# Kernel optimization log

Hardware: AMD Instinct MI355X
Metric: run time of the kernel (lower is better)

Reference implementation:

```python
import jax, jax.numpy as jnp
import numpy as np

HEADS = 8

def setup_inputs() -> dict:
    key = jax.random.key(0)
    ks = jax.random.split(key, 5)
    B, C, H, W = 2, 256, 64, 64
    dim = C
    x = jax.random.normal(ks[0], (B, C, H, W), dtype=jnp.float32)
    # Linear weights stored as [in, out] so y = x @ W + b
    w_qkv = jax.random.normal(ks[1], (dim, 3 * dim), dtype=jnp.float32) * (dim ** -0.5)
    b_qkv = jax.random.normal(ks[2], (3 * dim,), dtype=jnp.float32) * 0.02
    w_out = jax.random.normal(ks[3], (dim, dim), dtype=jnp.float32) * (dim ** -0.5)
    b_out = jax.random.normal(ks[4], (dim,), dtype=jnp.float32) * 0.02
    return {"x": x, "w_qkv": w_qkv, "b_qkv": b_qkv, "w_out": w_out, "b_out": b_out}

def reference(x, w_qkv, b_qkv, w_out, b_out):
    B, C, H, W = x.shape
    h = HEADS
    d = C // h
    scale = d ** -0.5
    # [B, C, H, W] -> [B, N, C]
    tokens = x.reshape(B, C, H * W).transpose(0, 2, 1)
    qkv = tokens @ w_qkv + b_qkv  # [B, N, 3C]
    q, k, v = jnp.split(qkv, 3, axis=-1)
    def to_heads(t):
        Bn, N, _ = t.shape
        return t.reshape(Bn, N, h, d).transpose(0, 2, 1, 3)  # [B, h, N, d]
    q, k, v = map(to_heads, (q, k, v))
    dots = jnp.einsum('bhnd,bhmd->bhnm', q, k) * scale  # [B, h, N, N]
    attn = jax.nn.softmax(dots, axis=-1)
    out = jnp.einsum('bhnm,bhmd->bhnd', attn, v)  # [B, h, N, d]
    out = out.transpose(0, 2, 1, 3).reshape(B, H * W, C)  # [B, N, C]
    out = out @ w_out + b_out
    return out.transpose(0, 2, 1).reshape(B, C, H, W)
```

## Files before the change

### kernel.cpp

```cpp
#include <hip/hip_runtime.h>

typedef __attribute__((ext_vector_type(8))) short s16x8;
typedef __attribute__((ext_vector_type(4))) float f32x4;
typedef __attribute__((ext_vector_type(16))) float f32x16;
typedef __attribute__((ext_vector_type(2))) unsigned u32x2;
typedef __attribute__((ext_vector_type(4))) unsigned u32x4;

#define MFMA32(a, b, c) __builtin_amdgcn_mfma_f32_16x16x32_bf16((a), (b), (c), 0, 0, 0)

#if __has_builtin(__builtin_amdgcn_mfma_f32_32x32x16_bf16)
#define MFMA3216(a, b, c) __builtin_amdgcn_mfma_f32_32x32x16_bf16((a), (b), (c), 0, 0, 0)
#else
#define MFMA3216(a, b, c) (c)
#endif

#if __has_builtin(__builtin_amdgcn_exp2f)
#define EXP2F(x) __builtin_amdgcn_exp2f(x)
#else
#define EXP2F(x) __exp2f(x)
#endif

#if __has_builtin(__builtin_amdgcn_rcpf)
#define RCPF(x) __builtin_amdgcn_rcpf(x)
#else
#define RCPF(x) (1.0f / (x))
#endif

#define SL2E 0.25507313f

__device__ __forceinline__ unsigned pkrne(float a, float b) {
  unsigned ua = __builtin_bit_cast(unsigned, a);
  unsigned ub = __builtin_bit_cast(unsigned, b);
  ua += 0x7FFFu + ((ua >> 16) & 1u);
  ub += 0x7FFFu + ((ub >> 16) & 1u);
  return __builtin_amdgcn_perm(ub, ua, 0x07060302u);
}

__device__ __forceinline__ unsigned pktrunc(float a, float b) {
  return __builtin_amdgcn_perm(__builtin_bit_cast(unsigned, b),
                               __builtin_bit_cast(unsigned, a), 0x07060302u);
}

__device__ __forceinline__ unsigned short bfr(float f) {
  unsigned u = __builtin_bit_cast(unsigned, f);
  u += 0x7FFFu + ((u >> 16) & 1u);
  return (unsigned short)(u >> 16);
}

__device__ __forceinline__ float bflo(unsigned u) {
  return __builtin_bit_cast(float, u << 16);
}
__device__ __forceinline__ float bfhi(unsigned u) {
  return __builtin_bit_cast(float, u & 0xFFFF0000u);
}

__device__ __forceinline__ u32x2 plswap(unsigned a, unsigned b) {
#if __has_builtin(__builtin_amdgcn_permlane32_swap)
  return __builtin_amdgcn_permlane32_swap(a, b, false, false);
#else
  unsigned sa = (unsigned)__shfl_xor((int)a, 32, 64);
  unsigned sb = (unsigned)__shfl_xor((int)b, 32, 64);
  bool hi = (threadIdx.x & 63) >= 32;
  u32x2 r;
  r.x = hi ? sb : a;
  r.y = hi ? b : sa;
  return r;
#endif
}

__device__ __forceinline__ void stage16(const ushort* g, ushort* l, int lane) {
#if __has_builtin(__builtin_amdgcn_global_load_lds)
  __builtin_amdgcn_global_load_lds(
      (__attribute__((address_space(1))) unsigned int*)(unsigned long long)(
          const void*)g,
      (__attribute__((address_space(3))) unsigned int*)(unsigned)(
          unsigned long long)(const void*)l,
      16, 0, 0);
#else
  *(uint4*)(l + lane * 8) = *(const uint4*)g;
#endif
}

__global__ __launch_bounds__(256) void prep_kernel(
    const float* __restrict__ x, const float* __restrict__ wqkv,
    const float* __restrict__ wout, ushort* __restrict__ xbf,
    ushort* __restrict__ wT, ushort* __restrict__ woT) {
  const int t = threadIdx.x;
  const int sub = t & 15, grp = t >> 4;
  const int id = blockIdx.x;
  const float* src;
  ushort* dst;
  int src_ld, k0, n0;
  float sc = 1.f;
  if (id < 512) {
    int mt = id & 63, kt = (id >> 6) & 3, b = id >> 8;
    src = x + (size_t)b * 256 * 4096;
    src_ld = 4096;
    dst = xbf + (size_t)b * 4096 * 256;
    k0 = kt * 64;
    n0 = mt * 64;
  } else if (id < 560) {
    int r = id - 512, nt = r % 12, kt = r / 12;
    src = wqkv;
    src_ld = 768;
    dst = wT;
    k0 = kt * 64;
    n0 = nt * 64;
    if (n0 < 256) sc = SL2E;
  } else {
    int r = id - 560, nt = r & 3, kt = r >> 2;
    src = wout;
    src_ld = 256;
    dst = woT;
    k0 = kt * 64;
    n0 = nt * 64;
  }
  const int k = k0 + grp * 4;
  const int n = n0 + sub * 4;
  unsigned d0[4], d1[4];
#pragma unroll
  for (int i = 0; i < 4; ++i) {
    float4 v = *(const float4*)(src + (size_t)(k + i) * src_ld + n);
    d0[i] = pkrne(v.x * sc, v.y * sc);
    d1[i] = pkrne(v.z * sc, v.w * sc);
  }
  u32x2 r0 = {__builtin_amdgcn_perm(d0[1], d0[0], 0x05040100u),
              __builtin_amdgcn_perm(d0[3], d0[2], 0x05040100u)};
  u32x2 r1 = {__builtin_amdgcn_perm(d0[1], d0[0], 0x07060302u),
              __builtin_amdgcn_perm(d0[3], d0[2], 0x07060302u)};
  u32x2 r2 = {__builtin_amdgcn_perm(d1[1], d1[0], 0x05040100u),
              __builtin_amdgcn_perm(d1[3], d1[2], 0x05040100u)};
  u32x2 r3 = {__builtin_amdgcn_perm(d1[1], d1[0], 0x07060302u),
              __builtin_amdgcn_perm(d1[3], d1[2], 0x07060302u)};
  *(u32x2*)(dst + (size_t)(n + 0) * 256 + k) = r0;
  *(u32x2*)(dst + (size_t)(n + 1) * 256 + k) = r1;
  *(u32x2*)(dst + (size_t)(n + 2) * 256 + k) = r2;
  *(u32x2*)(dst + (size_t)(n + 3) * 256 + k) = r3;
}

__global__ __launch_bounds__(256) void qkv_kernel(
    const ushort* __restrict__ xbf, const ushort* __restrict__ wT,
    const float* __restrict__ bq, ushort* __restrict__ QG,
    ushort* __restrict__ KG, ushort* __restrict__ VtG) {
  __shared__ __align__(16) ushort Wl[64][40];
  __shared__ __align__(16) ushort Xl[128][40];
  const int t0 = blockIdx.x * 128;
  const int n0 = blockIdx.y * 64;
  const int t = threadIdx.x;
  const int wid = t >> 6, lane = t & 63;
  const int wy = wid >> 1, wx = wid & 1;
  const int quad = lane >> 4, l16 = lane & 15;
  f32x4 acc[2][4] = {};
  const int wr = t >> 2, wsg = t & 3;
  for (int k0 = 0; k0 < 256; k0 += 32) {
    __syncthreads();
    *(uint4*)&Wl[wr][wsg * 8] =
        *(const uint4*)(wT + (size_t)(n0 + wr) * 256 + k0 + wsg * 8);
#pragma unroll
    for (int i = 0; i < 2; ++i) {
      int fid = t + 256 * i, row = fid >> 2, seg = fid & 3;
      *(uint4*)&Xl[row][seg * 8] =
          *(const uint4*)(xbf + (size_t)(t0 + row) * 256 + k0 + seg * 8);
    }
    __syncthreads();
    s16x8 wf[2], xf[4];
#pragma unroll
    for (int i = 0; i < 2; ++i)
      wf[i] = *(const s16x8*)&Wl[32 * wy + 16 * i + l16][quad * 8];
#pragma unroll
    for (int j = 0; j < 4; ++j)
      xf[j] = *(const s16x8*)&Xl[64 * wx + 16 * j + l16][quad * 8];
#pragma unroll
    for (int i = 0; i < 2; ++i)
#pragma unroll
      for (int j = 0; j < 4; ++j) acc[i][j] = MFMA32(wf[i], xf[j], acc[i][j]);
  }
  if (n0 < 256) {
#pragma unroll
    for (int i = 0; i < 2; ++i) {
      int nb = n0 + 32 * wy + 16 * i + 4 * quad;
      float4 b4 = *(const float4*)(bq + nb);
      float bx0 = b4.x * SL2E, bx1 = b4.y * SL2E, bx2 = b4.z * SL2E,
            bx3 = b4.w * SL2E;
      int h = ((nb & 255) >> 5);
      int dd0 = nb & 31;
#pragma unroll
      for (int j = 0; j < 4; ++j) {
        int tok = t0 + 64 * wx + 16 * j + l16;
        int b = tok >> 12, tokn = tok & 4095;
        u32x2 pk = {pkrne(acc[i][j][0] + bx0, acc[i][j][1] + bx1),
                    pkrne(acc[i][j][2] + bx2, acc[i][j][3] + bx3)};
        *(u32x2*)(QG + ((size_t)(b * 8 + h) * 4096 + tokn) * 32 + dd0) = pk;
      }
    }
  } else if (n0 < 512) {
#pragma unroll
    for (int i = 0; i < 2; ++i) {
      int nb = n0 + 32 * wy + 16 * i + 4 * quad;
      float4 b4 = *(const float4*)(bq + nb);
      float bx0 = b4.x, bx1 = b4.y, bx2 = b4.z, bx3 = b4.w;
      int h = ((nb & 255) >> 5);
      size_t fo = (size_t)i * 512 + (quad >> 1) * 256 + (quad & 1) * 4;
#pragma unroll
      for (int j = 0; j < 4; ++j) {
        int tok = t0 + 64 * wx + 16 * j + l16;
        int b = tok >> 12, tokn = tok & 4095;
        int tl = tokn >> 6, ss = (tokn >> 5) & 1, l5 = tokn & 31;
        u32x2 pk = {pkrne(acc[i][j][0] + bx0, acc[i][j][1] + bx1),
                    pkrne(acc[i][j][2] + bx2, acc[i][j][3] + bx3)};
        *(u32x2*)(KG + (size_t)(b * 8 + h) * 131072 + (size_t)tl * 2048 +
                  ss * 1024 + l5 * 8 + fo) = pk;
      }
    }
  } else {
#pragma unroll
    for (int i = 0; i < 2; ++i) {
      int nb = n0 + 32 * wy + 16 * i + 4 * quad;
      float4 b4 = *(const float4*)(bq + nb);
      float bb[4] = {b4.x, b4.y, b4.z, b4.w};
#pragma unroll
      for (int r = 0; r < 4; ++r) {
        int nn = nb + r - 512;
        int h = nn >> 5, d = nn & 31;
#pragma unroll
        for (int j = 0; j < 4; ++j) {
          int tok = t0 + 64 * wx + 16 * j + l16;
          int b = tok >> 12, tokn = tok & 4095;
          int tl = tokn >> 6, ss = (tokn >> 5) & 1;
          int hV = (tokn >> 4) & 1, hii = (tokn >> 3) & 1, e = tokn & 7;
          VtG[(size_t)(b * 8 + h) * 131072 + (size_t)tl * 2048 + ss * 1024 +
              hV * 512 + hii * 256 + d * 8 + e] = bfr(acc[i][j][r] + bb[r]);
        }
      }
    }
  }
}

struct AttnAcc {
  f32x16 o;
  f32x16 o_l;
};

__device__ __forceinline__ void softpv(const f32x16& S, const ushort* vhalf,
                                       int lane, f32x16& o, f32x16& o_l) {
  const s16x8 ones8 = {(short)0x3F80, (short)0x3F80, (short)0x3F80,
                       (short)0x3F80, (short)0x3F80, (short)0x3F80,
                       (short)0x3F80, (short)0x3F80};
  unsigned w8[8];
#pragma unroll
  for (int ii = 0; ii < 8; ++ii)
    w8[ii] = pktrunc(EXP2F(S[2 * ii]), EXP2F(S[2 * ii + 1]));
  u32x2 sw0 = plswap(w8[0], w8[2]);
  u32x2 sw1 = plswap(w8[1], w8[3]);
  u32x2 sw2 = plswap(w8[4], w8[6]);
  u32x2 sw3 = plswap(w8[5], w8[7]);
  u32x4 pa0 = {sw0.x, sw1.x, sw0.y, sw1.y};
  u32x4 pa1 = {sw2.x, sw3.x, sw2.y, sw3.y};
  const s16x8 pA0 = __builtin_bit_cast(s16x8, pa0);
  const s16x8 pA1 = __builtin_bit_cast(s16x8, pa1);
  const s16x8 va0 = *(const s16x8*)(vhalf + lane * 8);
  const s16x8 va1 = *(const s16x8*)(vhalf + 512 + lane * 8);
  o = MFMA3216(pA0, va0, o);
  o = MFMA3216(pA1, va1, o);
  o_l = MFMA3216(pA0, ones8, o_l);
  o_l = MFMA3216(pA1, ones8, o_l);
}

__global__ __launch_bounds__(256, 4) void attn_split(
    const ushort* __restrict__ QG, const ushort* __restrict__ KG,
    const ushort* __restrict__ VtG, ushort* __restrict__ OF0,
    ushort* __restrict__ OFb, float* __restrict__ LF) {
  __shared__ __align__(64) ushort KVs[3][4096];
  const int id = blockIdx.x;
  const int bh = (id & 7) * 2 + ((id >> 3) & 1);
  const int q0 = ((id >> 4) & 31) * 128;
  const int sp = id >> 9;
  const int kt0 = sp * 32;
  const int niter = 32;
  const int t = threadIdx.x;
  const int wid = t >> 6, lane = t & 63;
  const int l5 = lane & 31, hi = lane >> 5;
  const ushort* qp = QG + (size_t)bh * 4096 * 32;
  const ushort* kgp = KG + (size_t)bh * 131072 + (size_t)kt0 * 2048;
  const ushort* vgp = VtG + (size_t)bh * 131072 + (size_t)kt0 * 2048;
  const int qw = q0 + 32 * wid;
  const ushort* qrow = qp + (size_t)(qw + l5) * 32 + hi * 8;
  const s16x8 qf0 = *(const s16x8*)(qrow);
  const s16x8 qf1 = *(const s16x8*)(qrow + 16);
  const int kdst = wid * 512;
  const ushort* kpre = kgp + kdst + lane * 8;
  const ushort* vpre = vgp + kdst + lane * 8;
  stage16(kpre, &KVs[0][kdst], lane);
  stage16(vpre, &KVs[0][2048 + kdst], lane);
  kpre += 2048;
  vpre += 2048;
  __syncthreads();
  f32x16 o = {};
  f32x16 o_l = {};
  f32x16 S1p = {};
  int b = 0, bm1 = 2, bp1 = 1;
  const int lo8 = lane * 8;
  for (int i = 0; i < niter; ++i) {
    if (i + 1 < niter) {
      stage16(kpre, &KVs[bp1][kdst], lane);
      stage16(vpre, &KVs[bp1][2048 + kdst], lane);
      kpre += 2048;
      vpre += 2048;
    }
    const ushort* kb = &KVs[b][0];
    const s16x8 ka00 = *(const s16x8*)(kb + lo8);
    const s16x8 ka01 = *(const s16x8*)(kb + 512 + lo8);
    f32x16 S0 = {};
    S0 = MFMA3216(ka00, qf0, S0);
    S0 = MFMA3216(ka01, qf1, S0);
    if (i > 0) softpv(S1p, &KVs[bm1][2048 + 1024], lane, o, o_l);
    const s16x8 ka10 = *(const s16x8*)(kb + 1024 + lo8);
    const s16x8 ka11 = *(const s16x8*)(kb + 1536 + lo8);
    f32x16 S1 = {};
    S1 = MFMA3216(ka10, qf0, S1);
    S1 = MFMA3216(ka11, qf1, S1);
    softpv(S0, &KVs[b][2048], lane, o, o_l);
    S1p = S1;
    __syncthreads();
    bm1 = b;
    b = bp1;
    bp1 = (bp1 + 1 == 3) ? 0 : bp1 + 1;
  }
  softpv(S1p, &KVs[bm1][2048 + 1024], lane, o, o_l);
  ushort* OFs = (sp == 0) ? OF0 : OFb;
  float* LFs = LF + (size_t)sp * 65536;
#pragma unroll
  for (int r = 0; r < 16; ++r) {
    int q = qw + (r & 3) + 8 * (r >> 2) + 4 * hi;
    OFs[((size_t)bh * 4096 + q) * 32 + l5] = bfr(o[r]);
  }
  float lval = o_l[0];
#pragma unroll
  for (int r = 1; r < 16; ++r) lval = (l5 == r) ? o_l[r] : lval;
  if (l5 < 16)
    LFs[(size_t)bh * 4096 + qw + (l5 & 3) + 8 * (l5 >> 2) + 4 * hi] = lval;
}

__global__ __launch_bounds__(256) void proj_split(
    const ushort* __restrict__ OF0, const ushort* __restrict__ OFb,
    const float* __restrict__ LF, const ushort* __restrict__ woT,
    const float* __restrict__ bo, float* __restrict__ out) {
  __shared__ __align__(16) ushort Wl[64][40];
  __shared__ __align__(16) ushort Xl[64][40];
  const int t0 = blockIdx.x * 64;
  const int c0 = blockIdx.y * 64;
  const int t = threadIdx.x;
  const int wid = t >> 6, lane = t & 63;
  const int wy = wid >> 1, wx = wid & 1;
  const int quad = lane >> 4, l16 = lane & 15;
  f32x4 acc[2][2] = {};
  const int wr = t >> 2, wsg = t & 3;
  const int c8 = (t & 7) * 4;
  for (int k0 = 0; k0 < 256; k0 += 32) {
    __syncthreads();
    *(uint4*)&Wl[wr][wsg * 8] =
        *(const uint4*)(woT + (size_t)(c0 + wr) * 256 + k0 + wsg * 8);
    const int hh = k0 >> 5;
#pragma unroll
    for (int p = 0; p < 2; ++p) {
      int row = 32 * p + (t >> 3);
      int tok = t0 + row, bb = tok >> 12, tokn = tok & 4095;
      size_t ro = (size_t)(bb * 8 + hh) * 4096 + tokn;
      size_t oi = ro * 32 + c8;
      uint2 a0 = *(const uint2*)(OF0 + oi);
      uint2 a1 = *(const uint2*)(OFb + oi);
      float l = LF[ro] + LF[65536 + ro];
      float inv = RCPF(l);
      f32x4 s;
      s[0] = bflo(a0.x) + bflo(a1.x);
      s[1] = bfhi(a0.x) + bfhi(a1.x);
      s[2] = bflo(a0.y) + bflo(a1.y);
      s[3] = bfhi(a0.y) + bfhi(a1.y);
      s *= inv;
      u32x2 pk = {pkrne(s[0], s[1]), pkrne(s[2], s[3])};
      *(u32x2*)&Xl[row][c8] = pk;
    }
    __syncthreads();
    s16x8 wf[2], xf[2];
#pragma unroll
    for (int i = 0; i < 2; ++i)
      wf[i] = *(const s16x8*)&Wl[32 * wy + 16 * i + l16][quad * 8];
#pragma unroll
    for (int j = 0; j < 2; ++j)
      xf[j] = *(const s16x8*)&Xl[32 * wx + 16 * j + l16][quad * 8];
#pragma unroll
    for (int i = 0; i < 2; ++i)
#pragma unroll
      for (int j = 0; j < 2; ++j) acc[i][j] = MFMA32(wf[i], xf[j], acc[i][j]);
  }
#pragma unroll
  for (int i = 0; i < 2; ++i) {
    int cb = c0 + 32 * wy + 16 * i + 4 * quad;
    float4 b4 = *(const float4*)(bo + cb);
    float bb[4] = {b4.x, b4.y, b4.z, b4.w};
#pragma unroll
    for (int j = 0; j < 2; ++j) {
      int tok = t0 + 32 * wx + 16 * j + l16;
      int b = tok >> 12, tokn = tok & 4095;
#pragma unroll
      for (int r = 0; r < 4; ++r)
        out[((size_t)(b * 256 + cb + r)) * 4096 + tokn] = acc[i][j][r] + bb[r];
    }
  }
}

extern "C" void kernel_launch(void* const* d_in, const int* in_sizes, int n_in,
                              void* d_out, int out_size, void* d_ws, size_t ws_size,
                              hipStream_t stream) {
  (void)in_sizes; (void)n_in; (void)out_size; (void)ws_size;
  const float* x = (const float*)d_in[0];
  const float* wq = (const float*)d_in[1];
  const float* bq = (const float*)d_in[2];
  const float* wo = (const float*)d_in[3];
  const float* bo = (const float*)d_in[4];
  float* out = (float*)d_out;
  ushort* ws = (ushort*)d_ws;
  ushort* xbf = ws;
  ushort* OF0 = ws;
  ushort* QG  = ws + 2097152;
  ushort* KG  = ws + 4194304;
  ushort* VtG = ws + 6291456;
  ushort* wT  = ws + 8388608;
  ushort* woT = ws + 8585216;
  ushort* OFb = ws + 8650752;
  float* LF = (float*)(ws + 12845056);
  prep_kernel<<<576, 256, 0, stream>>>(x, wq, wo, xbf, wT, woT);
  qkv_kernel<<<dim3(64, 12), 256, 0, stream>>>(xbf, wT, bq, QG, KG, VtG);
  attn_split<<<1024, 256, 0, stream>>>(QG, KG, VtG, OF0, OFb, LF);
  proj_split<<<dim3(128, 4), 256, 0, stream>>>(OF0, OFb, LF, woT, bo, out);
}
```

Measured before the change: 136.6 us.

## Quad-buffer K/V tiles with explicit vmcnt waits and unrolled attention loop

Replaces the triple-buffered K/V loop with a 4-deep LDS ring, fully unrolled in groups of four so buffer indices are compile-time constants. Each step waits on the global loads with explicit s_waitcnt vmcnt counts and a raw s_barrier, which lets one stage of prefetch stay in flight across the barrier instead of draining everything at __syncthreads. It also raises wave priority around the QK MFMAs. In exchange, LDS use per block grows by a third, which may limit occupancy, and correctness now depends on the hand-written waitcnt values matching what stage16 actually issues.

```diff
diff --git a/kernel.cpp b/kernel.cpp
--- a/kernel.cpp
+++ b/kernel.cpp
@@ -236,11 +236,6 @@
   }
 }
 
-struct AttnAcc {
-  f32x16 o;
-  f32x16 o_l;
-};
-
 __device__ __forceinline__ void softpv(const f32x16& S, const ushort* vhalf,
                                        int lane, f32x16& o, f32x16& o_l) {
   const s16x8 ones8 = {(short)0x3F80, (short)0x3F80, (short)0x3F80,
@@ -266,17 +261,48 @@
   o_l = MFMA3216(pA1, ones8, o_l);
 }
 
+#define ATTN_STEP(CUR, PRV, SKEW, LAST)                                      \
+  {                                                                          \
+    if (!(LAST)) {                                                           \
+      stage16(kpre, &KVs[((CUR) + 1) & 3][kdst], lane);                      \
+      stage16(vpre, &KVs[((CUR) + 1) & 3][2048 + kdst], lane);               \
+      kpre += 2048;                                                          \
+      vpre += 2048;                                                          \
+      asm volatile("s_waitcnt vmcnt(2)" ::: "memory");                       \
+    } else {                                                                 \
+      asm volatile("s_waitcnt vmcnt(0)" ::: "memory");                       \
+    }                                                                        \
+    __builtin_amdgcn_sched_barrier(0);                                       \
+    __builtin_amdgcn_s_barrier();                                            \
+    __builtin_amdgcn_sched_barrier(0);                                       \
+    const ushort* kb = &KVs[(CUR)][0];                                       \
+    const s16x8 ka00 = *(const s16x8*)(kb + lo8);                            \
+    const s16x8 ka01 = *(const s16x8*)(kb + 512 + lo8);                      \
+    __builtin_amdgcn_s_setprio(1);                                           \
+    f32x16 S0 = MFMA3216(ka00, qf0, fz);                                     \
+    S0 = MFMA3216(ka01, qf1, S0);                                            \
+    __builtin_amdgcn_s_setprio(0);                                           \
+    if (SKEW) softpv(S1p, &KVs[(PRV)][2048 + 1024], lane, o, o_l);           \
+    const s16x8 ka10 = *(const s16x8*)(kb + 1024 + lo8);                     \
+    const s16x8 ka11 = *(const s16x8*)(kb + 1536 + lo8);                     \
+    __builtin_amdgcn_s_setprio(1);                                           \
+    f32x16 S1 = MFMA3216(ka10, qf0, fz);                                     \
+    S1 = MFMA3216(ka11, qf1, S1);                                            \
+    __builtin_amdgcn_s_setprio(0);                                           \
+    softpv(S0, &KVs[(CUR)][2048], lane, o, o_l);                             \
+    S1p = S1;                                                                \
+  }
+
 __global__ __launch_bounds__(256, 4) void attn_split(
     const ushort* __restrict__ QG, const ushort* __restrict__ KG,
     const ushort* __restrict__ VtG, ushort* __restrict__ OF0,
     ushort* __restrict__ OFb, float* __restrict__ LF) {
-  __shared__ __align__(64) ushort KVs[3][4096];
+  __shared__ __align__(64) ushort KVs[4][4096];
   const int id = blockIdx.x;
   const int bh = (id & 7) * 2 + ((id >> 3) & 1);
   const int q0 = ((id >> 4) & 31) * 128;
   const int sp = id >> 9;
   const int kt0 = sp * 32;
-  const int niter = 32;
   const int t = threadIdx.x;
   const int wid = t >> 6, lane = t & 63;
   const int l5 = lane & 31, hi = lane >> 5;
@@ -294,39 +320,26 @@
   stage16(vpre, &KVs[0][2048 + kdst], lane);
   kpre += 2048;
   vpre += 2048;
-  __syncthreads();
   f32x16 o = {};
   f32x16 o_l = {};
   f32x16 S1p = {};
-  int b = 0, bm1 = 2, bp1 = 1;
+  const f32x16 fz = {};
   const int lo8 = lane * 8;
-  for (int i = 0; i < niter; ++i) {
-    if (i + 1 < niter) {
-      stage16(kpre, &KVs[bp1][kdst], lane);
-      stage16(vpre, &KVs[bp1][2048 + kdst], lane);
-      kpre += 2048;
-      vpre += 2048;
-    }
-    const ushort* kb = &KVs[b][0];
-    const s16x8 ka00 = *(const s16x8*)(kb + lo8);
-    const s16x8 ka01 = *(const s16x8*)(kb + 512 + lo8);
-    f32x16 S0 = {};
-    S0 = MFMA3216(ka00, qf0, S0);
-    S0 = MFMA3216(ka01, qf1, S0);
-    if (i > 0) softpv(S1p, &KVs[bm1][2048 + 1024], lane, o, o_l);
-    const s16x8 ka10 = *(const s16x8*)(kb + 1024 + lo8);
-    const s16x8 ka11 = *(const s16x8*)(kb + 1536 + lo8);
-    f32x16 S1 = {};
-    S1 = MFMA3216(ka10, qf0, S1);
-    S1 = MFMA3216(ka11, qf1, S1);
-    softpv(S0, &KVs[b][2048], lane, o, o_l);
-    S1p = S1;
-    __syncthreads();
-    bm1 = b;
-    b = bp1;
-    bp1 = (bp1 + 1 == 3) ? 0 : bp1 + 1;
-  }
-  softpv(S1p, &KVs[bm1][2048 + 1024], lane, o, o_l);
+  ATTN_STEP(0, 3, false, false)
+  ATTN_STEP(1, 0, true, false)
+  ATTN_STEP(2, 1, true, false)
+  ATTN_STEP(3, 2, true, false)
+  for (int g = 1; g < 7; ++g) {
+    ATTN_STEP(0, 3, true, false)
+    ATTN_STEP(1, 0, true, false)
+    ATTN_STEP(2, 1, true, false)
+    ATTN_STEP(3, 2, true, false)
+  }
+  ATTN_STEP(0, 3, true, false)
+  ATTN_STEP(1, 0, true, false)
+  ATTN_STEP(2, 1, true, false)
+  ATTN_STEP(3, 2, true, true)
+  softpv(S1p, &KVs[3][2048 + 1024], lane, o, o_l);
   ushort* OFs = (sp == 0) ? OF0 : OFb;
   float* LFs = LF + (size_t)sp * 65536;
 #pragma unroll
```

Result: no change. 134.9 us (-1.2%).

## Pre-swizzle X and weights into fragment-tiled layout, use direct-to-LDS loads with double buffering

Applied to the files above, without the earlier changes.

The prep kernel now writes bf16 X and weight matrices in a tiled layout that matches the MFMA fragment order. This lets the QKV and projection GEMMs stage tiles with global_load_lds, and the QKV GEMM double-buffers them so the next k-slice loads during compute. The attention kernel drops from a triple-buffered software pipeline with a deferred softmax·V stage to a simpler double-buffered loop, unrolled two tiles per iteration. The aim is to cut register-staged LDS writes and padding overhead. The cost is less overlap inside each attention iteration.

```diff
diff --git a/kernel.cpp b/kernel.cpp
--- a/kernel.cpp
+++ b/kernel.cpp
@@ -81,6 +81,15 @@
 #endif
 }
 
+__device__ __forceinline__ size_t flX(int n, int k) {
+  return (size_t)(n >> 7) * 32768 + (size_t)(k >> 5) * 4096 +
+         ((n >> 4) & 7) * 512 + ((k >> 3) & 3) * 128 + (n & 15) * 8 + (k & 7);
+}
+__device__ __forceinline__ size_t flW(int n, int k) {
+  return (size_t)(n >> 6) * 16384 + (size_t)(k >> 5) * 2048 +
+         ((n >> 4) & 3) * 512 + ((k >> 3) & 3) * 128 + (n & 15) * 8 + (k & 7);
+}
+
 __global__ __launch_bounds__(256) void prep_kernel(
     const float* __restrict__ x, const float* __restrict__ wqkv,
     const float* __restrict__ wout, ushort* __restrict__ xbf,
@@ -91,14 +100,16 @@
   const float* src;
   ushort* dst;
   int src_ld, k0, n0;
+  bool isX = false;
   float sc = 1.f;
   if (id < 512) {
     int mt = id & 63, kt = (id >> 6) & 3, b = id >> 8;
     src = x + (size_t)b * 256 * 4096;
     src_ld = 4096;
-    dst = xbf + (size_t)b * 4096 * 256;
+    dst = xbf + (size_t)b * 1048576;
     k0 = kt * 64;
     n0 = mt * 64;
+    isX = true;
   } else if (id < 560) {
     int r = id - 512, nt = r % 12, kt = r / 12;
     src = wqkv;
@@ -132,48 +143,60 @@
               __builtin_amdgcn_perm(d1[3], d1[2], 0x05040100u)};
   u32x2 r3 = {__builtin_amdgcn_perm(d1[1], d1[0], 0x07060302u),
               __builtin_amdgcn_perm(d1[3], d1[2], 0x07060302u)};
-  *(u32x2*)(dst + (size_t)(n + 0) * 256 + k) = r0;
-  *(u32x2*)(dst + (size_t)(n + 1) * 256 + k) = r1;
-  *(u32x2*)(dst + (size_t)(n + 2) * 256 + k) = r2;
-  *(u32x2*)(dst + (size_t)(n + 3) * 256 + k) = r3;
+  if (isX) {
+    *(u32x2*)(dst + flX(n + 0, k)) = r0;
+    *(u32x2*)(dst + flX(n + 1, k)) = r1;
+    *(u32x2*)(dst + flX(n + 2, k)) = r2;
+    *(u32x2*)(dst + flX(n + 3, k)) = r3;
+  } else {
+    *(u32x2*)(dst + flW(n + 0, k)) = r0;
+    *(u32x2*)(dst + flW(n + 1, k)) = r1;
+    *(u32x2*)(dst + flW(n + 2, k)) = r2;
+    *(u32x2*)(dst + flW(n + 3, k)) = r3;
+  }
 }
 
 __global__ __launch_bounds__(256) void qkv_kernel(
     const ushort* __restrict__ xbf, const ushort* __restrict__ wT,
     const float* __restrict__ bq, ushort* __restrict__ QG,
     ushort* __restrict__ KG, ushort* __restrict__ VtG) {
-  __shared__ __align__(16) ushort Wl[64][40];
-  __shared__ __align__(16) ushort Xl[128][40];
+  __shared__ __align__(64) ushort WL[2][2048];
+  __shared__ __align__(64) ushort XL[2][4096];
   const int t0 = blockIdx.x * 128;
   const int n0 = blockIdx.y * 64;
   const int t = threadIdx.x;
   const int wid = t >> 6, lane = t & 63;
   const int wy = wid >> 1, wx = wid & 1;
   const int quad = lane >> 4, l16 = lane & 15;
+  const int lo8 = lane * 8;
   f32x4 acc[2][4] = {};
-  const int wr = t >> 2, wsg = t & 3;
-  for (int k0 = 0; k0 < 256; k0 += 32) {
+  const ushort* wsrc = wT + (size_t)blockIdx.y * 16384 + wid * 512 + lo8;
+  const ushort* xsrc = xbf + (size_t)blockIdx.x * 32768 + wid * 1024 + lo8;
+  stage16(wsrc, &WL[0][wid * 512], lane);
+  stage16(xsrc, &XL[0][wid * 1024], lane);
+  stage16(xsrc + 512, &XL[0][wid * 1024 + 512], lane);
+  __syncthreads();
+#pragma unroll
+  for (int ks = 0; ks < 8; ++ks) {
+    const int cur = ks & 1;
+    if (ks + 1 < 8) {
+      stage16(wsrc + (ks + 1) * 2048, &WL[cur ^ 1][wid * 512], lane);
+      stage16(xsrc + (size_t)(ks + 1) * 4096, &XL[cur ^ 1][wid * 1024], lane);
+      stage16(xsrc + (size_t)(ks + 1) * 4096 + 512,
+              &XL[cur ^ 1][wid * 1024 + 512], lane);
+    }
+    s16x8 wf[2], xf[4];
+#pragma unroll
+    for (int i = 0; i < 2; ++i)
+      wf[i] = *(const s16x8*)&WL[cur][(2 * wy + i) * 512 + lo8];
+#pragma unroll
+    for (int j = 0; j < 4; ++j)
+      xf[j] = *(const s16x8*)&XL[cur][(4 * wx + j) * 512 + lo8];
+#pragma unroll
+    for (int i = 0; i < 2; ++i)
+#pragma unroll
+      for (int j = 0; j < 4; ++j) acc[i][j] = MFMA32(wf[i], xf[j], acc[i][j]);
     __syncthreads();
-    *(uint4*)&Wl[wr][wsg * 8] =
-        *(const uint4*)(wT + (size_t)(n0 + wr) * 256 + k0 + wsg * 8);
-#pragma unroll
-    for (int i = 0; i < 2; ++i) {
-      int fid = t + 256 * i, row = fid >> 2, seg = fid & 3;
-      *(uint4*)&Xl[row][seg * 8] =
-          *(const uint4*)(xbf + (size_t)(t0 + row) * 256 + k0 + seg * 8);
-    }
-    __syncthreads();
-    s16x8 wf[2], xf[4];
-#pragma unroll
-    for (int i = 0; i < 2; ++i)
-      wf[i] = *(const s16x8*)&Wl[32 * wy + 16 * i + l16][quad * 8];
-#pragma unroll
-    for (int j = 0; j < 4; ++j)
-      xf[j] = *(const s16x8*)&Xl[64 * wx + 16 * j + l16][quad * 8];
-#pragma unroll
-    for (int i = 0; i < 2; ++i)
-#pragma unroll
-      for (int j = 0; j < 4; ++j) acc[i][j] = MFMA32(wf[i], xf[j], acc[i][j]);
   }
   if (n0 < 256) {
 #pragma unroll
@@ -236,13 +259,8 @@
   }
 }
 
-struct AttnAcc {
-  f32x16 o;
-  f32x16 o_l;
-};
-
-__device__ __forceinline__ void softpv(const f32x16& S, const ushort* vhalf,
-                                       int lane, f32x16& o, f32x16& o_l) {
+__device__ __forceinline__ void softpv(const f32x16& S, s16x8 va0, s16x8 va1,
+                                       f32x16& o, f32x16& o_l) {
   const s16x8 ones8 = {(short)0x3F80, (short)0x3F80, (short)0x3F80,
                        (short)0x3F80, (short)0x3F80, (short)0x3F80,
                        (short)0x3F80, (short)0x3F80};
@@ -258,38 +276,48 @@
   u32x4 pa1 = {sw2.x, sw3.x, sw2.y, sw3.y};
   const s16x8 pA0 = __builtin_bit_cast(s16x8, pa0);
   const s16x8 pA1 = __builtin_bit_cast(s16x8, pa1);
-  const s16x8 va0 = *(const s16x8*)(vhalf + lane * 8);
-  const s16x8 va1 = *(const s16x8*)(vhalf + 512 + lane * 8);
   o = MFMA3216(pA0, va0, o);
   o = MFMA3216(pA1, va1, o);
   o_l = MFMA3216(pA0, ones8, o_l);
   o_l = MFMA3216(pA1, ones8, o_l);
 }
 
+#define ATILE(BUF)                                                       \
+  {                                                                      \
+    const ushort* kb = &KVs[BUF][0];                                     \
+    const ushort* vb = &KVs[BUF][2048];                                  \
+    f32x16 S0 = MFMA3216(*(const s16x8*)(kb + lo8), qf0, fz);            \
+    S0 = MFMA3216(*(const s16x8*)(kb + 512 + lo8), qf1, S0);             \
+    softpv(S0, *(const s16x8*)(vb + lo8), *(const s16x8*)(vb + 512 + lo8), \
+           o, o_l);                                                      \
+    f32x16 S1 = MFMA3216(*(const s16x8*)(kb + 1024 + lo8), qf0, fz);     \
+    S1 = MFMA3216(*(const s16x8*)(kb + 1536 + lo8), qf1, S1);            \
+    softpv(S1, *(const s16x8*)(vb + 1024 + lo8),                         \
+           *(const s16x8*)(vb + 1536 + lo8), o, o_l);                    \
+  }
+
 __global__ __launch_bounds__(256, 4) void attn_split(
     const ushort* __restrict__ QG, const ushort* __restrict__ KG,
     const ushort* __restrict__ VtG, ushort* __restrict__ OF0,
     ushort* __restrict__ OFb, float* __restrict__ LF) {
-  __shared__ __align__(64) ushort KVs[3][4096];
+  __shared__ __align__(64) ushort KVs[2][4096];
   const int id = blockIdx.x;
   const int bh = (id & 7) * 2 + ((id >> 3) & 1);
   const int q0 = ((id >> 4) & 31) * 128;
   const int sp = id >> 9;
   const int kt0 = sp * 32;
-  const int niter = 32;
   const int t = threadIdx.x;
   const int wid = t >> 6, lane = t & 63;
   const int l5 = lane & 31, hi = lane >> 5;
+  const int lo8 = lane * 8;
   const ushort* qp = QG + (size_t)bh * 4096 * 32;
-  const ushort* kgp = KG + (size_t)bh * 131072 + (size_t)kt0 * 2048;
-  const ushort* vgp = VtG + (size_t)bh * 131072 + (size_t)kt0 * 2048;
   const int qw = q0 + 32 * wid;
   const ushort* qrow = qp + (size_t)(qw + l5) * 32 + hi * 8;
   const s16x8 qf0 = *(const s16x8*)(qrow);
   const s16x8 qf1 = *(const s16x8*)(qrow + 16);
   const int kdst = wid * 512;
-  const ushort* kpre = kgp + kdst + lane * 8;
-  const ushort* vpre = vgp + kdst + lane * 8;
+  const ushort* kpre = KG + (size_t)bh * 131072 + (size_t)kt0 * 2048 + kdst + lo8;
+  const ushort* vpre = VtG + (size_t)bh * 131072 + (size_t)kt0 * 2048 + kdst + lo8;
   stage16(kpre, &KVs[0][kdst], lane);
   stage16(vpre, &KVs[0][2048 + kdst], lane);
   kpre += 2048;
@@ -297,36 +325,23 @@
   __syncthreads();
   f32x16 o = {};
   f32x16 o_l = {};
-  f32x16 S1p = {};
-  int b = 0, bm1 = 2, bp1 = 1;
-  const int lo8 = lane * 8;
-  for (int i = 0; i < niter; ++i) {
-    if (i + 1 < niter) {
-      stage16(kpre, &KVs[bp1][kdst], lane);
-      stage16(vpre, &KVs[bp1][2048 + kdst], lane);
+  const f32x16 fz = {};
+  for (int p = 0; p < 16; ++p) {
+    stage16(kpre, &KVs[1][kdst], lane);
+    stage16(vpre, &KVs[1][2048 + kdst], lane);
+    kpre += 2048;
+    vpre += 2048;
+    ATILE(0)
+    __syncthreads();
+    if (p < 15) {
+      stage16(kpre, &KVs[0][kdst], lane);
+      stage16(vpre, &KVs[0][2048 + kdst], lane);
       kpre += 2048;
       vpre += 2048;
     }
-    const ushort* kb = &KVs[b][0];
-    const s16x8 ka00 = *(const s16x8*)(kb + lo8);
-    const s16x8 ka01 = *(const s16x8*)(kb + 512 + lo8);
-    f32x16 S0 = {};
-    S0 = MFMA3216(ka00, qf0, S0);
-    S0 = MFMA3216(ka01, qf1, S0);
-    if (i > 0) softpv(S1p, &KVs[bm1][2048 + 1024], lane, o, o_l);
-    const s16x8 ka10 = *(const s16x8*)(kb + 1024 + lo8);
-    const s16x8 ka11 = *(const s16x8*)(kb + 1536 + lo8);
-    f32x16 S1 = {};
-    S1 = MFMA3216(ka10, qf0, S1);
-    S1 = MFMA3216(ka11, qf1, S1);
-    softpv(S0, &KVs[b][2048], lane, o, o_l);
-    S1p = S1;
+    ATILE(1)
     __syncthreads();
-    bm1 = b;
-    b = bp1;
-    bp1 = (bp1 + 1 == 3) ? 0 : bp1 + 1;
-  }
-  softpv(S1p, &KVs[bm1][2048 + 1024], lane, o, o_l);
+  }
   ushort* OFs = (sp == 0) ? OF0 : OFb;
   float* LFs = LF + (size_t)sp * 65536;
 #pragma unroll
@@ -345,7 +360,7 @@
     const ushort* __restrict__ OF0, const ushort* __restrict__ OFb,
     const float* __restrict__ LF, const ushort* __restrict__ woT,
     const float* __restrict__ bo, float* __restrict__ out) {
-  __shared__ __align__(16) ushort Wl[64][40];
+  __shared__ __align__(64) ushort WL[2048];
   __shared__ __align__(16) ushort Xl[64][40];
   const int t0 = blockIdx.x * 64;
   const int c0 = blockIdx.y * 64;
@@ -353,13 +368,13 @@
   const int wid = t >> 6, lane = t & 63;
   const int wy = wid >> 1, wx = wid & 1;
   const int quad = lane >> 4, l16 = lane & 15;
+  const int lo8 = lane * 8;
   f32x4 acc[2][2] = {};
-  const int wr = t >> 2, wsg = t & 3;
   const int c8 = (t & 7) * 4;
+  const ushort* wsrc = woT + (size_t)blockIdx.y * 16384 + wid * 512 + lo8;
   for (int k0 = 0; k0 < 256; k0 += 32) {
     __syncthreads();
-    *(uint4*)&Wl[wr][wsg * 8] =
-        *(const uint4*)(woT + (size_t)(c0 + wr) * 256 + k0 + wsg * 8);
+    stage16(wsrc + (k0 >> 5) * 2048, &WL[wid * 512], lane);
     const int hh = k0 >> 5;
 #pragma unroll
     for (int p = 0; p < 2; ++p) {
@@ -384,7 +399,7 @@
     s16x8 wf[2], xf[2];
 #pragma unroll
     for (int i = 0; i < 2; ++i)
-      wf[i] = *(const s16x8*)&Wl[32 * wy + 16 * i + l16][quad * 8];
+      wf[i] = *(const s16x8*)&WL[(2 * wy + i) * 512 + lo8];
 #pragma unroll
     for (int j = 0; j < 2; ++j)
       xf[j] = *(const s16x8*)&Xl[32 * wx + 16 * j + l16][quad * 8];
```

Measured after the change: 134.7 us. No clear change (-1.4%).
